# Kernel tuning notes

Measured on AMD Instinct MI355X. Metric: run time of the kernel, lower is better.

The kernel has to match this reference:

```python
import jax, jax.numpy as jnp
import numpy as np

# Master-Slave MoE: dense shared 'master' expert Mlp applied to every token,
# plus num_experts 'slave' Mlp experts combined via top-k softmax gating,
# output = master(x) + sum_k gate_k * expert_k(x). Each Mlp: fc2(gelu(fc1(x))).

DIM = 512
HID = 4 * DIM
NUM_EXPERTS = 8
TOP_K = 2


def mlp(x, w1, b1, w2, b2):
    h = jax.nn.gelu(jnp.einsum('bnd,dh->bnh', x, w1) + b1)
    return jnp.einsum('bnh,hd->bnd', h, w2) + b2


def setup_inputs() -> dict:
    key = jax.random.key(0)
    ks = jax.random.split(key, 10)
    B, N = 4, 4096
    s1 = 1.0 / np.sqrt(DIM)
    s2 = 1.0 / np.sqrt(HID)
    return {
        'x': jax.random.normal(ks[0], (B, N, DIM), jnp.float32),
        'gate_w': jax.random.normal(ks[1], (DIM, NUM_EXPERTS), jnp.float32) * s1,
        'master_w1': jax.random.normal(ks[2], (DIM, HID), jnp.float32) * s1,
        'master_b1': jnp.zeros((HID,), jnp.float32),
        'master_w2': jax.random.normal(ks[3], (HID, DIM), jnp.float32) * s2,
        'master_b2': jnp.zeros((DIM,), jnp.float32),
        'expert_w1': jax.random.normal(ks[4], (NUM_EXPERTS, DIM, HID), jnp.float32) * s1,
        'expert_b1': jnp.zeros((NUM_EXPERTS, HID), jnp.float32),
        'expert_w2': jax.random.normal(ks[5], (NUM_EXPERTS, HID, DIM), jnp.float32) * s2,
        'expert_b2': jnp.zeros((NUM_EXPERTS, DIM), jnp.float32),
    }


def reference(x, gate_w, master_w1, master_b1, master_w2, master_b2,
              expert_w1, expert_b1, expert_w2, expert_b2):
    B, N, D = x.shape
    # Router: top-k softmax gating over experts
    logits = jnp.einsum('bnd,de->bne', x, gate_w)  # [B,N,E]
    topv, topi = jax.lax.top_k(logits, TOP_K)       # [B,N,K]
    gates_k = jax.nn.softmax(topv, axis=-1)         # [B,N,K]
    # dense gate matrix [B,N,E] (zeros for non-selected experts)
    gates = jnp.zeros_like(logits)
    gates = jnp.take_along_axis(gates, topi, axis=-1)  # noop to keep shape clarity
    gates = jnp.zeros_like(logits).at[
        jnp.arange(B)[:, None, None],
        jnp.arange(N)[None, :, None],
        topi].set(gates_k)

    # Master (shared) expert applied to all tokens
    master_out = mlp(x, master_w1, master_b1, master_w2, master_b2)

    # Slave experts: compute per-expert Mlp (vectorized over experts),
    # combine with gate weights. Gate is sparse (only top-k nonzero),
    # mathematically equal to token routing.
    h = jax.nn.gelu(jnp.einsum('bnd,edh->ebnh', x, expert_w1)
                    + expert_b1[:, None, None, :])          # [E,B,N,H]
    eo = jnp.einsum('ebnh,ehd->ebnd', h, expert_w2) \
         + expert_b2[:, None, None, :]                       # [E,B,N,D]
    slave_out = jnp.einsum('bne,ebnd->bnd', gates, eo)

    return master_out + slave_out
```

## Files before the change

kernel.cpp:

```cpp
#include <hip/hip_runtime.h>

#define DIM 512
#define HID 2048
#define NE 8

typedef _Float16 half8v __attribute__((ext_vector_type(8)));
typedef _Float16 half4v __attribute__((ext_vector_type(4)));
typedef float f32x4 __attribute__((ext_vector_type(4)));

__device__ __forceinline__ void gload16(const void* g, void* l) {
  __builtin_amdgcn_global_load_lds(
      (const __attribute__((address_space(1))) void*)g,
      (__attribute__((address_space(3))) void*)l, 16, 0, 0);
}

__global__ void k_transpose_cast9(const float* __restrict__ src_e,
                                  const float* __restrict__ src_m,
                                  _Float16* __restrict__ dst, int R, int C) {
  __shared__ _Float16 ts[64][66];
  int z = blockIdx.z;
  const float* src = (z == NE) ? src_m : src_e + (size_t)z * R * C;
  _Float16* d = dst + (size_t)z * R * C;
  int c0 = blockIdx.x * 64, r0 = blockIdx.y * 64;
  int t = threadIdx.x;
  int rr = t >> 4, cc = (t & 15) * 4;
  #pragma unroll
  for (int i = 0; i < 4; i++) {
    int row = rr + i * 16;
    float4 v = *(const float4*)&src[(size_t)(r0 + row) * C + c0 + cc];
    ts[row][cc + 0] = (_Float16)v.x; ts[row][cc + 1] = (_Float16)v.y;
    ts[row][cc + 2] = (_Float16)v.z; ts[row][cc + 3] = (_Float16)v.w;
  }
  __syncthreads();
  int cr = t >> 4, rb = (t & 15) * 4;
  #pragma unroll
  for (int i = 0; i < 4; i++) {
    int c = cr + i * 16;
    half4v o = { ts[rb + 0][c], ts[rb + 1][c], ts[rb + 2][c], ts[rb + 3][c] };
    *(half4v*)&d[(size_t)(c0 + c) * R + r0 + rb] = o;
  }
}

#define RT_TOK 16
__global__ void k_router(const float* __restrict__ x, const float* __restrict__ gw,
                         _Float16* __restrict__ xb,
                         int* __restrict__ counts, int* __restrict__ perm,
                         float* __restrict__ pgate, int T) {
  __shared__ float xs[RT_TOK][520];
  __shared__ float gwt[8][520];
  __shared__ float lg[RT_TOK][8];
  int t = threadIdx.x;
  int tk0 = blockIdx.x * RT_TOK;
  for (int i = t; i < DIM * NE; i += 128) {
    int k = i >> 3, e = i & 7;
    gwt[e][k] = gw[i];
  }
  for (int i = t; i < RT_TOK * (DIM / 4); i += 128) {
    int row = i >> 7; int c4 = i & 127;
    float4 v = *(const float4*)&x[(size_t)(tk0 + row) * DIM + c4 * 4];
    xs[row][c4 * 4 + 0] = v.x; xs[row][c4 * 4 + 1] = v.y;
    xs[row][c4 * 4 + 2] = v.z; xs[row][c4 * 4 + 3] = v.w;
    half4v h = { (_Float16)v.x, (_Float16)v.y, (_Float16)v.z, (_Float16)v.w };
    *(half4v*)&xb[(size_t)(tk0 + row) * DIM + c4 * 4] = h;
  }
  __syncthreads();
  int tok = t >> 3, e = t & 7;
  float acc = 0.f;
  for (int k = 0; k < DIM; k += 4) {
    float4 xv = *(const float4*)&xs[tok][k];
    float4 wv = *(const float4*)&gwt[e][k];
    acc += xv.x * wv.x + xv.y * wv.y + xv.z * wv.z + xv.w * wv.w;
  }
  lg[tok][e] = acc;
  __syncthreads();
  if (t < RT_TOK) {
    float v0 = -1e30f, v1 = -1e30f; int i0 = 0, i1 = 0;
    #pragma unroll
    for (int j = 0; j < 8; j++) { float v = lg[t][j]; if (v > v0) { v0 = v; i0 = j; } }
    #pragma unroll
    for (int j = 0; j < 8; j++) { if (j == i0) continue; float v = lg[t][j]; if (v > v1) { v1 = v; i1 = j; } }
    float g0 = 1.f / (1.f + __expf(v1 - v0));
    float g1 = 1.f - g0;
    int token = tk0 + t;
    int p0 = atomicAdd(&counts[i0], 1);
    perm[i0 * T + p0] = token; pgate[i0 * T + p0] = g0;
    int p1 = atomicAdd(&counts[i1], 1);
    perm[i1 * T + p1] = token; pgate[i1 * T + p1] = g1;
  }
}


#define STG 24576
#define BOFF 16384

__device__ __forceinline__ void compute_tile(const char* base,
                                             int wm, int wn, int rb,
                                             f32x4 acc[4][4]) {
  const char* ab = base;
  const char* bb = base + BOFF;
  half8v af[4], bf[4];
  #pragma unroll
  for (int mi = 0; mi < 4; mi++)
    af[mi] = *(const half8v*)(ab + ((wm + mi * 16) << 6) + rb);
  #pragma unroll
  for (int ni = 0; ni < 4; ni++)
    bf[ni] = *(const half8v*)(bb + ((wn + ni * 16) << 6) + rb);
  #pragma unroll
  for (int mi = 0; mi < 4; mi++)
    #pragma unroll
    for (int ni = 0; ni < 4; ni++)
      acc[mi][ni] = __builtin_amdgcn_mfma_f32_16x16x32_f16(af[mi], bf[ni], acc[mi][ni], 0, 0, 0);
}

template<int K, int MODE>
__global__ __launch_bounds__(512) void k_gemm(
    const _Float16* __restrict__ A,
    const _Float16* __restrict__ Bt,
    const float* __restrict__ ebias,
    const float* __restrict__ mbias,
    const int* __restrict__ counts,
    const int* __restrict__ perm,
    const float* __restrict__ pgate,
    _Float16* __restrict__ hout,
    float* __restrict__ out,
    int T) {
  constexpr int N = (MODE == 0) ? HID : DIM;
  constexpr int KT = K / 32;
  int e = blockIdx.z;
  bool isM = (e == NE);
  int count = isM ? T : counts[e];
  int m0 = blockIdx.x * 256;
  if (m0 >= count) return;
  int n0 = blockIdx.y * 128;
  int hbase = 0;
  if (isM) hbase = 2 * T;
  else for (int i = 0; i < e; i++) hbase += counts[i];
  const _Float16* Be = Bt + (size_t)e * N * K;
  const float* be = isM ? mbias : ebias + (size_t)e * N;

  __shared__ _Float16 S[3 * STG / 2];

  int t = threadIdx.x;
  int lane = t & 63;
  int wid = t >> 6;
  int wm = (wid & 3) * 64, wn = (wid >> 2) * 64;

  const char* aSrc0; const char* aSrc1; const char* bSrc0;
  {
    int r0a = t >> 2,        cg0 = (t & 3) ^ ((r0a + (r0a >> 2)) & 3);
    int r1a = r0a + 128,     cg1 = (t & 3) ^ ((r1a + (r1a >> 2)) & 3);
    int pos0 = m0 + r0a; int pr0 = pos0 < count ? pos0 : count - 1;
    int pos1 = m0 + r1a; int pr1 = pos1 < count ? pos1 : count - 1;
    int arow0, arow1;
    if (MODE == 0) {
      arow0 = isM ? pr0 : perm[e * T + pr0];
      arow1 = isM ? pr1 : perm[e * T + pr1];
    } else {
      arow0 = hbase + pr0; arow1 = hbase + pr1;
    }
    aSrc0 = (const char*)(A + (size_t)arow0 * K) + cg0 * 16;
    aSrc1 = (const char*)(A + (size_t)arow1 * K) + cg1 * 16;
    bSrc0 = (const char*)(Be + (size_t)(n0 + r0a) * K) + cg0 * 16;
  }

  int qa = (lane >> 4) ^ (((lane & 3) + ((lane >> 2) & 3)) & 3);
  int rb = ((lane & 15) << 6) + (qa << 4);

  f32x4 acc[4][4] = {};

  char* p0 = (char*)S;
  char* p1 = (char*)S + STG;
  char* p2 = (char*)S + 2 * STG;

#define STAGE_TO(base, off) do { \
    gload16(aSrc0 + (off), (base) + t * 16); \
    gload16(aSrc1 + (off), (base) + t * 16 + 8192); \
    gload16(bSrc0 + (off), (base) + BOFF + t * 16); \
  } while (0)

  STAGE_TO(p0, 0);
  STAGE_TO(p1, 64);

  for (int kt = 0; kt < KT; ++kt) {
    if (kt + 1 < KT) { asm volatile("s_waitcnt vmcnt(3)" ::: "memory"); }
    else             { asm volatile("s_waitcnt vmcnt(0)" ::: "memory"); }
    __builtin_amdgcn_s_barrier();
    if (kt + 2 < KT) STAGE_TO(p2, (kt + 2) * 64);
    __builtin_amdgcn_s_setprio(1);
    compute_tile(p0, wm, wn, rb, acc);
    __builtin_amdgcn_s_setprio(0);
    char* tp = p0; p0 = p1; p1 = p2; p2 = tp;
  }
#undef STAGE_TO

  int cl = lane & 15, rh = (lane >> 4) * 4;
  float bv[4];
  #pragma unroll
  for (int ni = 0; ni < 4; ni++) bv[ni] = be[n0 + wn + ni * 16 + cl];
  #pragma unroll
  for (int mi = 0; mi < 4; mi++) {
    #pragma unroll
    for (int r = 0; r < 4; r++) {
      int pos = m0 + wm + mi * 16 + rh + r;
      if (pos >= count) continue;
      int orow; float g = 1.f;
      if (MODE == 0) orow = hbase + pos;
      else {
        orow = isM ? pos : perm[e * T + pos];
        if (!isM) g = pgate[e * T + pos];
      }
      #pragma unroll
      for (int ni = 0; ni < 4; ni++) {
        float v = acc[mi][ni][r] + bv[ni];
        int col = n0 + wn + ni * 16 + cl;
        if (MODE == 0) {
          float ge = v / (1.f + __expf(-1.5957691216057308f * (v + 0.044715f * v * v * v)));
          hout[(size_t)orow * HID + col] = (_Float16)ge;
        } else {
          unsafeAtomicAdd(&out[(size_t)orow * DIM + col], g * v);
        }
      }
    }
  }
}

extern "C" void kernel_launch(void* const* d_in, const int* in_sizes, int n_in,
                              void* d_out, int out_size, void* d_ws, size_t ws_size,
                              hipStream_t stream) {
  const float* x         = (const float*)d_in[0];
  const float* gate_w    = (const float*)d_in[1];
  const float* master_w1 = (const float*)d_in[2];
  const float* master_b1 = (const float*)d_in[3];
  const float* master_w2 = (const float*)d_in[4];
  const float* master_b2 = (const float*)d_in[5];
  const float* expert_w1 = (const float*)d_in[6];
  const float* expert_b1 = (const float*)d_in[7];
  const float* expert_w2 = (const float*)d_in[8];
  const float* expert_b2 = (const float*)d_in[9];
  float* out = (float*)d_out;
  int T = in_sizes[0] / DIM;

  char* p = (char*)d_ws;
  _Float16* xb   = (_Float16*)p; p += (size_t)T * DIM * 2;
  _Float16* wb1t = (_Float16*)p; p += (size_t)9 * HID * DIM * 2;
  _Float16* wb2t = (_Float16*)p; p += (size_t)9 * DIM * HID * 2;
  int*   counts  = (int*)p;      p += 256;
  int*   perm    = (int*)p;      p += (size_t)8 * T * 4;
  float* pgate   = (float*)p;    p += (size_t)8 * T * 4;
  _Float16* hbuf = (_Float16*)p; p += (size_t)3 * T * HID * 2;

  hipMemsetAsync(counts, 0, 64, stream);
  hipMemsetAsync(out, 0, (size_t)T * DIM * 4, stream);

  k_router<<<T / RT_TOK, 128, 0, stream>>>(x, gate_w, xb, counts, perm, pgate, T);

  k_transpose_cast9<<<dim3(HID / 64, DIM / 64, 9), 256, 0, stream>>>(
      expert_w1, master_w1, wb1t, DIM, HID);
  k_transpose_cast9<<<dim3(DIM / 64, HID / 64, 9), 256, 0, stream>>>(
      expert_w2, master_w2, wb2t, HID, DIM);

  k_gemm<DIM, 0><<<dim3(T / 256, HID / 128, 9), 512, 0, stream>>>(
      xb, wb1t, expert_b1, master_b1, counts, perm, nullptr,
      hbuf, nullptr, T);
  k_gemm<HID, 2><<<dim3(T / 256, DIM / 128, 9), 512, 0, stream>>>(
      hbuf, wb2t, expert_b2, master_b2, counts, perm, pgate,
      nullptr, out, T);
}
```

Baseline: 722.1 us.

## Enlarge GEMM tiles to 256x256 with K=64 steps and double-buffered LDS

Changes the grouped GEMM block tile from 256x128 to 256x256 with each wave computing a 128x64 sub-tile, and raises the K step from 32 to 64. It replaces the triple-buffered 24 KB LDS stages with two 64 KB buffers in dynamic shared memory, using a new XOR swizzle over 128-byte rows. The aim is more MFMA work per byte staged and fewer barriers per K. In exchange, accumulator register use doubles, occupancy drops to one block per CU, and the second GEMM launches fewer blocks (N=512 gives only 2 column tiles), which risks idle CUs.

```diff
diff --git a/kernel.cpp b/kernel.cpp
--- a/kernel.cpp
+++ b/kernel.cpp
@@ -90,30 +90,8 @@
 }
 
 
-#define STG 24576
-#define BOFF 16384
-
-__device__ __forceinline__ void compute_tile(const char* base,
-                                             int wm, int wn, int rb,
-                                             f32x4 acc[4][4]) {
-  const char* ab = base;
-  const char* bb = base + BOFF;
-  half8v af[4], bf[4];
-  #pragma unroll
-  for (int mi = 0; mi < 4; mi++)
-    af[mi] = *(const half8v*)(ab + ((wm + mi * 16) << 6) + rb);
-  #pragma unroll
-  for (int ni = 0; ni < 4; ni++)
-    bf[ni] = *(const half8v*)(bb + ((wn + ni * 16) << 6) + rb);
-  #pragma unroll
-  for (int mi = 0; mi < 4; mi++)
-    #pragma unroll
-    for (int ni = 0; ni < 4; ni++)
-      acc[mi][ni] = __builtin_amdgcn_mfma_f32_16x16x32_f16(af[mi], bf[ni], acc[mi][ni], 0, 0, 0);
-}
-
 template<int K, int MODE>
-__global__ __launch_bounds__(512) void k_gemm(
+__global__ __launch_bounds__(512, 1) void k_gemm(
     const _Float16* __restrict__ A,
     const _Float16* __restrict__ Bt,
     const float* __restrict__ ebias,
@@ -125,80 +103,116 @@
     float* __restrict__ out,
     int T) {
   constexpr int N = (MODE == 0) ? HID : DIM;
-  constexpr int KT = K / 32;
+  constexpr int KT = K / 64;
+  extern __shared__ char S[];
   int e = blockIdx.z;
   bool isM = (e == NE);
   int count = isM ? T : counts[e];
   int m0 = blockIdx.x * 256;
   if (m0 >= count) return;
-  int n0 = blockIdx.y * 128;
+  int n0 = blockIdx.y * 256;
   int hbase = 0;
   if (isM) hbase = 2 * T;
   else for (int i = 0; i < e; i++) hbase += counts[i];
   const _Float16* Be = Bt + (size_t)e * N * K;
   const float* be = isM ? mbias : ebias + (size_t)e * N;
 
-  __shared__ _Float16 S[3 * STG / 2];
-
   int t = threadIdx.x;
   int lane = t & 63;
   int wid = t >> 6;
-  int wm = (wid & 3) * 64, wn = (wid >> 2) * 64;
-
-  const char* aSrc0; const char* aSrc1; const char* bSrc0;
+  int wm = (wid >> 2) * 128;
+  int wn = (wid & 3) * 64;
+
+  int srow = t >> 3;
+  int schunk = (t & 7) ^ (srow & 7);
+  const char *aP0, *aP1, *aP2, *aP3, *bP0, *bP1, *bP2, *bP3;
   {
-    int r0a = t >> 2,        cg0 = (t & 3) ^ ((r0a + (r0a >> 2)) & 3);
-    int r1a = r0a + 128,     cg1 = (t & 3) ^ ((r1a + (r1a >> 2)) & 3);
-    int pos0 = m0 + r0a; int pr0 = pos0 < count ? pos0 : count - 1;
-    int pos1 = m0 + r1a; int pr1 = pos1 < count ? pos1 : count - 1;
-    int arow0, arow1;
+    int r0 = srow, r1 = 64 + srow, r2 = 128 + srow, r3 = 192 + srow;
+    int p0 = m0 + r0; p0 = p0 < count ? p0 : count - 1;
+    int p1 = m0 + r1; p1 = p1 < count ? p1 : count - 1;
+    int p2 = m0 + r2; p2 = p2 < count ? p2 : count - 1;
+    int p3 = m0 + r3; p3 = p3 < count ? p3 : count - 1;
+    int a0, a1, a2, a3;
     if (MODE == 0) {
-      arow0 = isM ? pr0 : perm[e * T + pr0];
-      arow1 = isM ? pr1 : perm[e * T + pr1];
+      a0 = isM ? p0 : perm[e * T + p0];
+      a1 = isM ? p1 : perm[e * T + p1];
+      a2 = isM ? p2 : perm[e * T + p2];
+      a3 = isM ? p3 : perm[e * T + p3];
     } else {
-      arow0 = hbase + pr0; arow1 = hbase + pr1;
-    }
-    aSrc0 = (const char*)(A + (size_t)arow0 * K) + cg0 * 16;
-    aSrc1 = (const char*)(A + (size_t)arow1 * K) + cg1 * 16;
-    bSrc0 = (const char*)(Be + (size_t)(n0 + r0a) * K) + cg0 * 16;
-  }
-
-  int qa = (lane >> 4) ^ (((lane & 3) + ((lane >> 2) & 3)) & 3);
-  int rb = ((lane & 15) << 6) + (qa << 4);
-
-  f32x4 acc[4][4] = {};
-
-  char* p0 = (char*)S;
-  char* p1 = (char*)S + STG;
-  char* p2 = (char*)S + 2 * STG;
-
-#define STAGE_TO(base, off) do { \
-    gload16(aSrc0 + (off), (base) + t * 16); \
-    gload16(aSrc1 + (off), (base) + t * 16 + 8192); \
-    gload16(bSrc0 + (off), (base) + BOFF + t * 16); \
+      a0 = hbase + p0; a1 = hbase + p1; a2 = hbase + p2; a3 = hbase + p3;
+    }
+    aP0 = (const char*)(A + (size_t)a0 * K) + schunk * 16;
+    aP1 = (const char*)(A + (size_t)a1 * K) + schunk * 16;
+    aP2 = (const char*)(A + (size_t)a2 * K) + schunk * 16;
+    aP3 = (const char*)(A + (size_t)a3 * K) + schunk * 16;
+    bP0 = (const char*)(Be + (size_t)(n0 + r0) * K) + schunk * 16;
+    bP1 = (const char*)(Be + (size_t)(n0 + r1) * K) + schunk * 16;
+    bP2 = (const char*)(Be + (size_t)(n0 + r2) * K) + schunk * 16;
+    bP3 = (const char*)(Be + (size_t)(n0 + r3) * K) + schunk * 16;
+  }
+
+  int l15 = lane & 15, l4 = lane >> 4, l7 = lane & 7;
+  int roff0 = l15 * 128 + ((l4 ^ l7) << 4);
+  int roff1 = l15 * 128 + (((4 + l4) ^ l7) << 4);
+
+  f32x4 acc[8][4] = {};
+
+  char* buf0 = S;
+  char* buf1 = S + 65536;
+
+#define STAGE(base, ktile) do { \
+    const int off_ = (ktile) * 128; \
+    gload16(aP0 + off_, (base) + t * 16); \
+    gload16(aP1 + off_, (base) + 8192 + t * 16); \
+    gload16(aP2 + off_, (base) + 16384 + t * 16); \
+    gload16(aP3 + off_, (base) + 24576 + t * 16); \
+    gload16(bP0 + off_, (base) + 32768 + t * 16); \
+    gload16(bP1 + off_, (base) + 40960 + t * 16); \
+    gload16(bP2 + off_, (base) + 49152 + t * 16); \
+    gload16(bP3 + off_, (base) + 57344 + t * 16); \
   } while (0)
 
-  STAGE_TO(p0, 0);
-  STAGE_TO(p1, 64);
-
+  STAGE(buf0, 0);
   for (int kt = 0; kt < KT; ++kt) {
-    if (kt + 1 < KT) { asm volatile("s_waitcnt vmcnt(3)" ::: "memory"); }
-    else             { asm volatile("s_waitcnt vmcnt(0)" ::: "memory"); }
     __builtin_amdgcn_s_barrier();
-    if (kt + 2 < KT) STAGE_TO(p2, (kt + 2) * 64);
+    if (kt + 1 < KT) {
+      STAGE((kt & 1) ? buf0 : buf1, kt + 1);
+      asm volatile("s_waitcnt vmcnt(8)" ::: "memory");
+    } else {
+      asm volatile("s_waitcnt vmcnt(0)" ::: "memory");
+    }
+    __builtin_amdgcn_sched_barrier(0);
+    __builtin_amdgcn_s_barrier();
+    const char* base = (kt & 1) ? buf1 : buf0;
+    const char* ab = base;
+    const char* bb = base + 32768;
     __builtin_amdgcn_s_setprio(1);
-    compute_tile(p0, wm, wn, rb, acc);
+    #pragma unroll
+    for (int kk = 0; kk < 2; ++kk) {
+      int ro = kk ? roff1 : roff0;
+      half8v af[8], bf[4];
+      #pragma unroll
+      for (int mi = 0; mi < 8; mi++)
+        af[mi] = *(const half8v*)(ab + (wm + mi * 16) * 128 + ro);
+      #pragma unroll
+      for (int ni = 0; ni < 4; ni++)
+        bf[ni] = *(const half8v*)(bb + (wn + ni * 16) * 128 + ro);
+      #pragma unroll
+      for (int mi = 0; mi < 8; mi++)
+        #pragma unroll
+        for (int ni = 0; ni < 4; ni++)
+          acc[mi][ni] = __builtin_amdgcn_mfma_f32_16x16x32_f16(af[mi], bf[ni], acc[mi][ni], 0, 0, 0);
+    }
     __builtin_amdgcn_s_setprio(0);
-    char* tp = p0; p0 = p1; p1 = p2; p2 = tp;
-  }
-#undef STAGE_TO
-
-  int cl = lane & 15, rh = (lane >> 4) * 4;
+  }
+#undef STAGE
+
+  int cl = l15, rh = l4 * 4;
   float bv[4];
   #pragma unroll
   for (int ni = 0; ni < 4; ni++) bv[ni] = be[n0 + wn + ni * 16 + cl];
   #pragma unroll
-  for (int mi = 0; mi < 4; mi++) {
+  for (int mi = 0; mi < 8; mi++) {
     #pragma unroll
     for (int r = 0; r < 4; r++) {
       int pos = m0 + wm + mi * 16 + rh + r;
@@ -249,6 +263,11 @@
   float* pgate   = (float*)p;    p += (size_t)8 * T * 4;
   _Float16* hbuf = (_Float16*)p; p += (size_t)3 * T * HID * 2;
 
+  (void)hipFuncSetAttribute((const void*)&k_gemm<DIM, 0>,
+                            hipFuncAttributeMaxDynamicSharedMemorySize, 131072);
+  (void)hipFuncSetAttribute((const void*)&k_gemm<HID, 2>,
+                            hipFuncAttributeMaxDynamicSharedMemorySize, 131072);
+
   hipMemsetAsync(counts, 0, 64, stream);
   hipMemsetAsync(out, 0, (size_t)T * DIM * 4, stream);
 
@@ -259,10 +278,10 @@
   k_transpose_cast9<<<dim3(DIM / 64, HID / 64, 9), 256, 0, stream>>>(
       expert_w2, master_w2, wb2t, HID, DIM);
 
-  k_gemm<DIM, 0><<<dim3(T / 256, HID / 128, 9), 512, 0, stream>>>(
+  k_gemm<DIM, 0><<<dim3(T / 256, HID / 256, 9), 512, 131072, stream>>>(
       xb, wb1t, expert_b1, master_b1, counts, perm, nullptr,
       hbuf, nullptr, T);
-  k_gemm<HID, 2><<<dim3(T / 256, DIM / 128, 9), 512, 0, stream>>>(
+  k_gemm<HID, 2><<<dim3(T / 256, DIM / 256, 9), 512, 131072, stream>>>(
       hbuf, wb2t, expert_b2, master_b2, counts, perm, pgate,
       nullptr, out, T);
 }
```

Result: no change. 717.3 us (-0.7%).
